# Kernel optimization log

Hardware: AMD Instinct MI355X
Metric: run time of the kernel (lower is better)

The kernel has to match this reference:

```python
import jax, jax.numpy as jnp
import numpy as np

D_IN = 1024
D_OUT = 1024
NUM_HEADS = 16
HEAD_DIM = D_OUT // NUM_HEADS
SEQ = 2048
BATCH = 2


def setup_inputs() -> dict:
    key = jax.random.key(0)
    k1, k2, k3 = jax.random.split(key, 3)
    x = jax.random.normal(k1, (BATCH, SEQ, D_IN), dtype=jnp.float32)
    w_qkv = jax.random.normal(k2, (3 * D_OUT, D_IN), dtype=jnp.float32) * (1.0 / np.sqrt(D_IN))
    w_proj = jax.random.normal(k3, (D_OUT, D_OUT), dtype=jnp.float32) * (1.0 / np.sqrt(D_OUT))
    b_proj = jnp.zeros((D_OUT,), dtype=jnp.float32)
    return {"x": x, "w_qkv": w_qkv, "w_proj": w_proj, "b_proj": b_proj}


def reference(x, w_qkv, w_proj, b_proj):
    B, S, _ = x.shape
    # QKV projection (no bias, qkv_bias=False)
    qkv = x @ w_qkv.T                              # [B,S,3*D]
    qkv = qkv.reshape(B, S, 3, NUM_HEADS, HEAD_DIM)
    q = qkv[:, :, 0].transpose(0, 2, 1, 3)          # [B,H,S,hd]
    k = qkv[:, :, 1].transpose(0, 2, 1, 3)
    v = qkv[:, :, 2].transpose(0, 2, 1, 3)
    scores = jnp.einsum('bhqd,bhkd->bhqk', q, k)    # [B,H,S,S]
    causal = jnp.triu(jnp.ones((S, S), dtype=bool), k=1)
    scores = jnp.where(causal, -jnp.inf, scores)
    weights = jax.nn.softmax(scores / np.sqrt(HEAD_DIM), axis=-1)
    ctx = jnp.einsum('bhqk,bhkd->bhqd', weights, v)  # [B,H,S,hd]
    ctx = ctx.transpose(0, 2, 1, 3).reshape(B, S, D_OUT)
    return ctx @ w_proj.T + b_proj
```

## Files before the change

kernel.cpp:

```cpp
#include <hip/hip_runtime.h>
#include <hip/hip_bf16.h>
#include <stdint.h>

#define NHEAD 16
#define HDIM  64
#define SEQ   2048
#define BATCH 2

typedef __attribute__((ext_vector_type(8))) short          s16x8;
typedef __attribute__((ext_vector_type(4))) short          s16x4;
typedef __attribute__((ext_vector_type(4))) float          f32x4;
typedef __attribute__((ext_vector_type(8))) unsigned short u16x8;
typedef __attribute__((ext_vector_type(4))) unsigned short u16x4;

__device__ __forceinline__ unsigned short f2b(float f) {
  union { float f; unsigned u; } x; x.f = f;
  unsigned r = x.u + 0x7fffu + ((x.u >> 16) & 1u);
  return (unsigned short)(r >> 16);
}
__device__ __forceinline__ float b2f(unsigned short b) {
  union { unsigned u; float f; } x; x.u = ((unsigned)b) << 16;
  return x.f;
}

__device__ __forceinline__ void gload_lds16(const void* g, void* l) {
  __builtin_amdgcn_global_load_lds((const __attribute__((address_space(1))) void*)g,
                                   (__attribute__((address_space(3))) void*)l,
                                   16, 0, 0);
}

#define SWZ(a) ((a) ^ ((((a) >> 7) & 7) << 4))

__global__ __launch_bounds__(256) void cvt3(
    const float* __restrict__ a, unsigned short* __restrict__ oa, int na,
    const float* __restrict__ b, unsigned short* __restrict__ ob, int nb,
    const float* __restrict__ c, unsigned short* __restrict__ oc) {
  int idx = (blockIdx.x * 256 + threadIdx.x) * 4;
  const float* in; unsigned short* out;
  if (idx < na)            { in = a; out = oa; }
  else if (idx < na + nb)  { in = b; out = ob; idx -= na; }
  else                     { in = c; out = oc; idx -= na + nb; }
  float4 v = *(const float4*)(in + idx);
  u16x4 o;
  o[0] = f2b(v.x); o[1] = f2b(v.y); o[2] = f2b(v.z); o[3] = f2b(v.w);
  *(u16x4*)(out + idx) = o;
}

template <int EPI>
__global__ __launch_bounds__(256) void gemm_bt(
    const unsigned short* __restrict__ A,
    const unsigned short* __restrict__ B,
    int M, int N, int K,
    unsigned short* __restrict__ oq,
    unsigned short* __restrict__ ok,
    unsigned short* __restrict__ ov,
    float* __restrict__ out,
    const float* __restrict__ bias) {
  __shared__ unsigned short As[128 * 64];
  __shared__ unsigned short Bs[128 * 64];

  const int ntiles = N >> 7;
  const int mb = blockIdx.x / ntiles;
  const int nb = blockIdx.x % ntiles;
  const int mbase = mb << 7, nbase = nb << 7;

  const int tid  = threadIdx.x;
  const int lane = tid & 63;
  const int wid  = tid >> 6;
  const int wr   = (wid >> 1) * 64;
  const int wc   = (wid & 1) * 64;

  f32x4 acc[4][4];
  for (int r = 0; r < 4; ++r)
    for (int c = 0; c < 4; ++c) acc[r][c] = (f32x4){0.f, 0.f, 0.f, 0.f};

  const int rowA = lane >> 3;
  const int kbs  = ((lane & 7) * 16) ^ (rowA << 4);
  const size_t strideA = (size_t)K * 2;

  for (int kt = 0; kt < K; kt += 64) {
    for (int it = 0; it < 4; ++it) {
      int c   = wid * 4 + it;
      int row = c * 8 + rowA;
      gload_lds16((const char*)A + (size_t)(mbase + row) * strideA + (size_t)kt * 2 + kbs,
                  (char*)As + c * 1024 + (lane & 7) * 16);
      gload_lds16((const char*)B + (size_t)(nbase + row) * strideA + (size_t)kt * 2 + kbs,
                  (char*)Bs + c * 1024 + (lane & 7) * 16);
    }
    __syncthreads();
    const int sw = (lane & 7) << 4;
    for (int ks = 0; ks < 2; ++ks) {
      const int colb = ks * 64 + (lane >> 4) * 16;
      s16x8 af[4], bf[4];
      for (int r = 0; r < 4; ++r)
        af[r] = *(const s16x8*)((const char*)As + (wr + r * 16 + (lane & 15)) * 128 + (colb ^ sw));
      for (int c = 0; c < 4; ++c)
        bf[c] = *(const s16x8*)((const char*)Bs + (wc + c * 16 + (lane & 15)) * 128 + (colb ^ sw));
      for (int r = 0; r < 4; ++r)
        for (int c = 0; c < 4; ++c)
          acc[r][c] = __builtin_amdgcn_mfma_f32_16x16x32_bf16(af[r], bf[c], acc[r][c], 0, 0, 0);
    }
    __syncthreads();
  }

  for (int r = 0; r < 4; ++r) {
    for (int c = 0; c < 4; ++c) {
      const int n = nbase + wc + c * 16 + (lane & 15);
      for (int i = 0; i < 4; ++i) {
        const int m = mbase + wr + r * 16 + (lane >> 4) * 4 + i;
        float v = acc[r][c][i];
        if (EPI == 0) {
          int b = m >> 11, s = m & (SEQ - 1);
          int which = n >> 10, rr = n & 1023;
          int h = rr >> 6, d = rr & (HDIM - 1);
          if (which == 0)
            oq[(((size_t)b * NHEAD + h) * SEQ + s) * HDIM + d] = f2b(v);
          else if (which == 1)
            ok[(((size_t)b * NHEAD + h) * SEQ + s) * HDIM + d] = f2b(v);
          else
            ov[(((size_t)b * NHEAD + h) * HDIM + d) * SEQ + s] = f2b(v);
        } else {
          out[(size_t)m * N + n] = v + bias[n];
        }
      }
    }
  }
}

__global__ __launch_bounds__(256, 4) void flash_attn(
    const unsigned short* __restrict__ Qb,
    const unsigned short* __restrict__ Kb,
    const unsigned short* __restrict__ Vb,
    unsigned short* __restrict__ ctx) {
  const int bsw  = (int)blockIdx.x;
  const int lin  = ((bsw & 7) << 6) + (bsw >> 3);
  const int bh   = lin >> 4;
  const int pair = lin & 15;
  const int b    = bh >> 4;
  const int h    = bh & (NHEAD - 1);

  const unsigned short* Qh  = Qb + (size_t)bh * SEQ * HDIM;
  const char*           Khc = (const char*)(Kb + (size_t)bh * SEQ * HDIM);
  const char*           Vtc = (const char*)(Vb + (size_t)bh * HDIM * SEQ);

  const int tid = threadIdx.x, lane = tid & 63, wid = tid >> 6;
  const int g = lane >> 4, q = lane & 15;

  __shared__ unsigned short Ks[2][64 * 64];
  __shared__ unsigned short Vt[2][64 * 64];
  __shared__ unsigned short Ps[4][16 * 64];

  const int vy0   = (wid * 2) * 1024 + lane * 16;
  const int vrow0 = vy0 >> 7;
  const int vsw0  = ((vy0 & 127) ^ ((vrow0 & 7) << 4));
  const int vy1   = vy0 + 1024;
  const int vrow1 = vy1 >> 7;
  const int vsw1  = ((vy1 & 127) ^ ((vrow1 & 7) << 4));

  for (int pass = 0; pass < 2; ++pass) {
    const int qt    = pass ? pair : 31 - pair;
    const int qbase = qt * 64;

    s16x8 qf[2];
    {
      const int qrow = qbase + wid * 16 + q;
      for (int ks = 0; ks < 2; ++ks) {
        u16x8 raw = *(const u16x8*)&Qh[(size_t)qrow * HDIM + ks * 32 + g * 8];
        s16x8 qv;
        for (int j = 0; j < 8; ++j) qv[j] = (short)f2b(b2f(raw[j]) * 0.125f);
        qf[ks] = qv;
      }
    }

    float l4[4] = {0.f, 0.f, 0.f, 0.f};
    f32x4 o[4];
    for (int c = 0; c < 4; ++c) o[c] = (f32x4){0.f, 0.f, 0.f, 0.f};

    {
      for (int it = 0; it < 2; ++it) {
        const int x = (wid * 2 + it) * 1024 + lane * 16;
        gload_lds16(Khc + SWZ(x), (char*)Ks[0] + x);
      }
      gload_lds16(Vtc + (size_t)vrow0 * (SEQ * 2) + vsw0, (char*)Vt[0] + vy0);
      gload_lds16(Vtc + (size_t)vrow1 * (SEQ * 2) + vsw1, (char*)Vt[0] + vy1);
    }
    __syncthreads();

    for (int kt = 0; kt <= qt; ++kt) {
      const int cur = kt & 1, nxt = cur ^ 1;

      if (kt < qt) {
        const char* ksrc = Khc + (size_t)(kt + 1) * 8192;
        for (int it = 0; it < 2; ++it) {
          const int x = (wid * 2 + it) * 1024 + lane * 16;
          gload_lds16(ksrc + SWZ(x), (char*)Ks[nxt] + x);
        }
        const size_t vco = (size_t)(kt + 1) * 128;
        gload_lds16(Vtc + (size_t)vrow0 * (SEQ * 2) + vco + vsw0, (char*)Vt[nxt] + vy0);
        gload_lds16(Vtc + (size_t)vrow1 * (SEQ * 2) + vco + vsw1, (char*)Vt[nxt] + vy1);
      }

      f32x4 sa[4];
      for (int c = 0; c < 4; ++c) sa[c] = (f32x4){0.f, 0.f, 0.f, 0.f};
      for (int ks = 0; ks < 2; ++ks) {
        const int kb2 = ks * 64 + g * 16;
        for (int c = 0; c < 4; ++c) {
          const int row = c * 16 + q;
          const int a   = row * 128 + kb2;
          s16x8 kb8 = *(const s16x8*)((const char*)Ks[cur] + (a ^ ((row & 7) << 4)));
          sa[c] = __builtin_amdgcn_mfma_f32_16x16x32_bf16(kb8, qf[ks], sa[c], 0, 0, 0);
        }
      }

      if (kt == qt) {
        const int q_rel = wid * 16 + q;
        for (int c = 0; c < 4; ++c) {
          for (int i = 0; i < 4; ++i) {
            const int key_rel = c * 16 + g * 4 + i;
            if (key_rel > q_rel) sa[c][i] = -1e30f;
          }
        }
      }

      for (int c = 0; c < 4; ++c) {
        const float p0 = __expf(sa[c][0]);
        const float p1 = __expf(sa[c][1]);
        const float p2 = __expf(sa[c][2]);
        const float p3 = __expf(sa[c][3]);
        l4[0] += p0; l4[1] += p1; l4[2] += p2; l4[3] += p3;
        union { unsigned u[2]; s16x4 v; } pk;
        asm("v_cvt_pk_bf16_f32 %0, %1, %2" : "=v"(pk.u[0]) : "v"(p0), "v"(p1));
        asm("v_cvt_pk_bf16_f32 %0, %1, %2" : "=v"(pk.u[1]) : "v"(p2), "v"(p3));
        const int a2 = (q * 128 + c * 32 + g * 8) ^ ((q & 7) << 4);
        *(s16x4*)((char*)Ps[wid] + a2) = pk.v;
      }
      __builtin_amdgcn_sched_barrier(0);

      for (int ks = 0; ks < 2; ++ks) {
        const int kb2 = ks * 64 + g * 16;
        const int paa = q * 128 + kb2;
        s16x8 pa = *(const s16x8*)((const char*)Ps[wid] + (paa ^ ((q & 7) << 4)));
        for (int c = 0; c < 4; ++c) {
          const int row = c * 16 + q;
          const int a   = row * 128 + kb2;
          s16x8 vb8 = *(const s16x8*)((const char*)Vt[cur] + (a ^ ((row & 7) << 4)));
          o[c] = __builtin_amdgcn_mfma_f32_16x16x32_bf16(pa, vb8, o[c], 0, 0, 0);
        }
      }

      __syncthreads();
    }

    float lsum = (l4[0] + l4[1]) + (l4[2] + l4[3]);
    lsum += __shfl_xor(lsum, 16);
    lsum += __shfl_xor(lsum, 32);
    for (int i = 0; i < 4; ++i) {
      const int qi   = g * 4 + i;
      const float li = __shfl(lsum, qi);
      const float nv = 1.f / li;
      const int row  = qbase + wid * 16 + qi;
      for (int c = 0; c < 4; ++c) {
        const int col = h * HDIM + c * 16 + q;
        ctx[((size_t)b * SEQ + row) * (NHEAD * HDIM) + col] = f2b(o[c][i] * nv);
      }
    }
  }
}

extern "C" void kernel_launch(void* const* d_in, const int* in_sizes, int n_in,
                              void* d_out, int out_size, void* d_ws, size_t ws_size,
                              hipStream_t stream) {
  const float* x      = (const float*)d_in[0];
  const float* w_qkv  = (const float*)d_in[1];
  const float* w_proj = (const float*)d_in[2];
  const float* b_proj = (const float*)d_in[3];
  float* out = (float*)d_out;

  char* ws = (char*)d_ws;
  unsigned short* xb     = (unsigned short*)(ws);
  unsigned short* wqkvb  = (unsigned short*)(ws + 8388608);
  unsigned short* wprojb = (unsigned short*)(ws + 14680064);
  unsigned short* qb     = (unsigned short*)(ws + 16777216);
  unsigned short* kb     = (unsigned short*)(ws + 25165824);
  unsigned short* vb     = (unsigned short*)(ws + 33554432);
  unsigned short* ctx    = (unsigned short*)(ws + 41943040);

  cvt3<<<dim3(8192), dim3(256), 0, stream>>>(
      x, xb, 4096 * 1024, w_qkv, wqkvb, 3072 * 1024, w_proj, wprojb);

  gemm_bt<0><<<dim3(768), dim3(256), 0, stream>>>(
      xb, wqkvb, 4096, 3072, 1024, qb, kb, vb, (float*)nullptr, (const float*)nullptr);

  flash_attn<<<dim3(512), dim3(256), 0, stream>>>(qb, kb, vb, ctx);

  gemm_bt<1><<<dim3(256), dim3(256), 0, stream>>>(
      ctx, wprojb, 4096, 1024, 1024,
      (unsigned short*)nullptr, (unsigned short*)nullptr, (unsigned short*)nullptr,
      out, b_proj);
}
```

Before: 115.1 us.

## Double the attention key tile to 128 and halve occupancy bound

After: 119.8 us. +4.1%, slower.

```diff
diff --git a/kernel.cpp b/kernel.cpp
--- a/kernel.cpp
+++ b/kernel.cpp
@@ -127,7 +127,7 @@
   }
 }
 
-__global__ __launch_bounds__(256, 4) void flash_attn(
+__global__ __launch_bounds__(256, 2) void flash_attn(
     const unsigned short* __restrict__ Qb,
     const unsigned short* __restrict__ Kb,
     const unsigned short* __restrict__ Vb,
@@ -146,20 +146,17 @@
   const int tid = threadIdx.x, lane = tid & 63, wid = tid >> 6;
   const int g = lane >> 4, q = lane & 15;
 
-  __shared__ unsigned short Ks[2][64 * 64];
-  __shared__ unsigned short Vt[2][64 * 64];
-  __shared__ unsigned short Ps[4][16 * 64];
-
-  const int vy0   = (wid * 2) * 1024 + lane * 16;
-  const int vrow0 = vy0 >> 7;
-  const int vsw0  = ((vy0 & 127) ^ ((vrow0 & 7) << 4));
-  const int vy1   = vy0 + 1024;
-  const int vrow1 = vy1 >> 7;
-  const int vsw1  = ((vy1 & 127) ^ ((vrow1 & 7) << 4));
+  __shared__ unsigned short Ks[2][128 * 64];
+  __shared__ unsigned short Vt[2][64 * 128];
+  __shared__ unsigned short Ps[4][16 * 128];
+
+  char* const PsW = (char*)Ps[wid];
+  const int qsw = (q & 7) << 4;
 
   for (int pass = 0; pass < 2; ++pass) {
-    const int qt    = pass ? pair : 31 - pair;
-    const int qbase = qt * 64;
+    const int qt     = pass ? pair : 31 - pair;
+    const int qbase  = qt * 64;
+    const int nsteps = (qt + 2) >> 1;
 
     s16x8 qf[2];
     {
@@ -167,7 +164,7 @@
       for (int ks = 0; ks < 2; ++ks) {
         u16x8 raw = *(const u16x8*)&Qh[(size_t)qrow * HDIM + ks * 32 + g * 8];
         s16x8 qv;
-        for (int j = 0; j < 8; ++j) qv[j] = (short)f2b(b2f(raw[j]) * 0.125f);
+        for (int j2 = 0; j2 < 8; ++j2) qv[j2] = (short)f2b(b2f(raw[j2]) * 0.125f);
         qf[ks] = qv;
       }
     }
@@ -176,53 +173,51 @@
     f32x4 o[4];
     for (int c = 0; c < 4; ++c) o[c] = (f32x4){0.f, 0.f, 0.f, 0.f};
 
-    {
-      for (int it = 0; it < 2; ++it) {
-        const int x = (wid * 2 + it) * 1024 + lane * 16;
-        gload_lds16(Khc + SWZ(x), (char*)Ks[0] + x);
-      }
-      gload_lds16(Vtc + (size_t)vrow0 * (SEQ * 2) + vsw0, (char*)Vt[0] + vy0);
-      gload_lds16(Vtc + (size_t)vrow1 * (SEQ * 2) + vsw1, (char*)Vt[0] + vy1);
+    for (int it = 0; it < 4; ++it) {
+      const int x = (wid * 4 + it) * 1024 + lane * 16;
+      gload_lds16(Khc + SWZ(x), (char*)Ks[0] + x);
+      const int d  = x >> 8;
+      const int cb = (x & 255) ^ ((d & 7) << 4);
+      gload_lds16(Vtc + (size_t)d * (SEQ * 2) + cb, (char*)Vt[0] + x);
     }
     __syncthreads();
 
-    for (int kt = 0; kt <= qt; ++kt) {
-      const int cur = kt & 1, nxt = cur ^ 1;
-
-      if (kt < qt) {
-        const char* ksrc = Khc + (size_t)(kt + 1) * 8192;
-        for (int it = 0; it < 2; ++it) {
-          const int x = (wid * 2 + it) * 1024 + lane * 16;
-          gload_lds16(ksrc + SWZ(x), (char*)Ks[nxt] + x);
-        }
-        const size_t vco = (size_t)(kt + 1) * 128;
-        gload_lds16(Vtc + (size_t)vrow0 * (SEQ * 2) + vco + vsw0, (char*)Vt[nxt] + vy0);
-        gload_lds16(Vtc + (size_t)vrow1 * (SEQ * 2) + vco + vsw1, (char*)Vt[nxt] + vy1);
-      }
-
-      f32x4 sa[4];
-      for (int c = 0; c < 4; ++c) sa[c] = (f32x4){0.f, 0.f, 0.f, 0.f};
+    for (int s = 0; s < nsteps; ++s) {
+      const int cur = s & 1, nxt = cur ^ 1;
+
+      if (s + 1 < nsteps) {
+        for (int it = 0; it < 4; ++it) {
+          const int x = (wid * 4 + it) * 1024 + lane * 16;
+          gload_lds16(Khc + (size_t)(s + 1) * 16384 + SWZ(x), (char*)Ks[nxt] + x);
+          const int d  = x >> 8;
+          const int cb = (x & 255) ^ ((d & 7) << 4);
+          gload_lds16(Vtc + (size_t)d * (SEQ * 2) + (size_t)(s + 1) * 256 + cb,
+                      (char*)Vt[nxt] + x);
+        }
+      }
+
+      f32x4 sa[8];
+      for (int c = 0; c < 8; ++c) sa[c] = (f32x4){0.f, 0.f, 0.f, 0.f};
       for (int ks = 0; ks < 2; ++ks) {
         const int kb2 = ks * 64 + g * 16;
-        for (int c = 0; c < 4; ++c) {
+        for (int c = 0; c < 8; ++c) {
           const int row = c * 16 + q;
-          const int a   = row * 128 + kb2;
-          s16x8 kb8 = *(const s16x8*)((const char*)Ks[cur] + (a ^ ((row & 7) << 4)));
+          s16x8 kb8 = *(const s16x8*)((const char*)Ks[cur] + ((row * 128 + kb2) ^ qsw));
           sa[c] = __builtin_amdgcn_mfma_f32_16x16x32_bf16(kb8, qf[ks], sa[c], 0, 0, 0);
         }
       }
 
-      if (kt == qt) {
-        const int q_rel = wid * 16 + q;
-        for (int c = 0; c < 4; ++c) {
+      if (s == nsteps - 1) {
+        const int qg = qbase + wid * 16 + q;
+        for (int c = 0; c < 8; ++c) {
           for (int i = 0; i < 4; ++i) {
-            const int key_rel = c * 16 + g * 4 + i;
-            if (key_rel > q_rel) sa[c][i] = -1e30f;
+            const int kg = s * 128 + c * 16 + g * 4 + i;
+            if (kg > qg) sa[c][i] = -1e30f;
           }
         }
       }
 
-      for (int c = 0; c < 4; ++c) {
+      for (int c = 0; c < 8; ++c) {
         const float p0 = __expf(sa[c][0]);
         const float p1 = __expf(sa[c][1]);
         const float p2 = __expf(sa[c][2]);
@@ -231,19 +226,17 @@
         union { unsigned u[2]; s16x4 v; } pk;
         asm("v_cvt_pk_bf16_f32 %0, %1, %2" : "=v"(pk.u[0]) : "v"(p0), "v"(p1));
         asm("v_cvt_pk_bf16_f32 %0, %1, %2" : "=v"(pk.u[1]) : "v"(p2), "v"(p3));
-        const int a2 = (q * 128 + c * 32 + g * 8) ^ ((q & 7) << 4);
-        *(s16x4*)((char*)Ps[wid] + a2) = pk.v;
+        const int a2 = (q * 256 + c * 32 + g * 8) ^ qsw;
+        *(s16x4*)(PsW + a2) = pk.v;
       }
       __builtin_amdgcn_sched_barrier(0);
 
-      for (int ks = 0; ks < 2; ++ks) {
+      for (int ks = 0; ks < 4; ++ks) {
         const int kb2 = ks * 64 + g * 16;
-        const int paa = q * 128 + kb2;
-        s16x8 pa = *(const s16x8*)((const char*)Ps[wid] + (paa ^ ((q & 7) << 4)));
+        s16x8 pa = *(const s16x8*)(PsW + ((q * 256 + kb2) ^ qsw));
         for (int c = 0; c < 4; ++c) {
           const int row = c * 16 + q;
-          const int a   = row * 128 + kb2;
-          s16x8 vb8 = *(const s16x8*)((const char*)Vt[cur] + (a ^ ((row & 7) << 4)));
+          s16x8 vb8 = *(const s16x8*)((const char*)Vt[cur] + ((row * 256 + kb2) ^ qsw));
           o[c] = __builtin_amdgcn_mfma_f32_16x16x32_bf16(pa, vb8, o[c], 0, 0, 0);
         }
       }
```
